# Optimization experiments

Hardware: AMD Instinct MI355X
Metric: run time of the kernel (lower is better)

The kernel has to match this reference:

```python
import jax, jax.numpy as jnp
import numpy as np


def setup_inputs() -> dict:
    key = jax.random.key(0)
    kq, kk, kv = jax.random.split(key, 3)
    B, S, D = 4, 4096, 128
    return {
        "q_proj": jax.random.normal(kq, (B, S, D), dtype=jnp.float32),
        "k_proj": jax.random.normal(kk, (B, S, D), dtype=jnp.float32),
        "v_proj": jax.random.normal(kv, (B, S, D), dtype=jnp.float32),
    }


def reference(q_proj, k_proj, v_proj):
    # Block-wise online softmax in the original is mathematically exact
    # full (non-causal) scaled dot-product attention.
    d = q_proj.shape[-1]
    scale = 1.0 / jnp.sqrt(jnp.asarray(d, dtype=q_proj.dtype))
    logits = jnp.einsum('bqd,bkd->bqk', q_proj, k_proj) * scale  # [B,S,S]
    attn = jax.nn.softmax(logits, axis=-1)
    return jnp.einsum('bqk,bkd->bqd', attn, v_proj)
```

## Files before the change

### kernel.cpp

```cpp
#include <hip/hip_runtime.h>
#include <hip/hip_bf16.h>
#include <stdint.h>

#define Bn 4
#define Sn 4096
#define Dn 128
#define SCALE ((float)(0.08838834764831843 * 1.4426950408889634))

typedef __attribute__((ext_vector_type(8)))  short short8;
typedef __attribute__((ext_vector_type(4)))  short short4v;
typedef __attribute__((ext_vector_type(4)))  float f32x4;
typedef __attribute__((ext_vector_type(16))) float f32x16;
typedef __attribute__((ext_vector_type(2)))  uint32_t uint2v;

__device__ __forceinline__ uint32_t bfround(float f){
  union { float f; uint32_t u; } a; a.f = f;
  return a.u + 0x7FFFu + ((a.u >> 16) & 1u);
}
__device__ __forceinline__ uint32_t f2bf2(float lo, float hi){
  return (bfround(hi) & 0xFFFF0000u) | (bfround(lo) >> 16);
}
__device__ __forceinline__ uint32_t f2bf2_fast(float lo, float hi){
  const uint32_t a = __float_as_uint(lo) + 0x8000u;
  const uint32_t b = __float_as_uint(hi) + 0x8000u;
  return __builtin_amdgcn_perm(b, a, 0x07060302u);
}
__device__ __forceinline__ float bf2f(short s){
  union { uint32_t u; float f; } a; a.u = ((uint32_t)(unsigned short)s) << 16; return a.f;
}
__device__ __forceinline__ float fexp2(float x){
#if __has_builtin(__builtin_amdgcn_exp2f)
  return __builtin_amdgcn_exp2f(x);
#else
  return exp2f(x);
#endif
}

__device__ __forceinline__ void gload16(const void* g, void* l){
  __builtin_amdgcn_global_load_lds(
      (const __attribute__((address_space(1))) unsigned int*)g,
      (__attribute__((address_space(3))) unsigned int*)l, 16, 0, 0);
}

__global__ void prep_kernel(const float* __restrict__ k, const float* __restrict__ v,
                            short* __restrict__ kb, short* __restrict__ vt){
  const int bid = blockIdx.x;
  const int t   = threadIdx.x;
  if (bid < 2048){
    const int i = bid*256 + t;
    const f32x4 val = ((const f32x4*)k)[i];
    uint2v o;
    o[0] = f2bf2(val[0], val[1]);
    o[1] = f2bf2(val[2], val[3]);
    *(uint2v*)(kb + 4*(size_t)i) = o;
  } else {
    __shared__ float tile[64][65];
    const int vb = bid - 2048;
    const int s0 = (vb & 63) * 64;
    const int d0 = ((vb >> 6) & 1) * 64;
    const int b  = vb >> 7;
#pragma unroll
    for (int i=0;i<16;++i){
      int lin = i*256 + t;
      int r = lin >> 6, c = lin & 63;
      tile[r][c] = v[((size_t)(b*Sn + s0 + r))*Dn + d0 + c];
    }
    __syncthreads();
#pragma unroll
    for (int i=0;i<2;++i){
      int lin = i*256 + t;
      int r = lin >> 3;
      int u = lin & 7;
      union { uint32_t w[4]; short8 s; } pk;
#pragma unroll
      for (int p=0;p<4;++p){
        int x0 = u*8 + 2*p, x1 = x0 + 1;
        int k0 = (x0 & ~15) | ((x0 & 3) | (((x0>>2)&1)<<3) | (((x0>>3)&1)<<2));
        int k1 = (x1 & ~15) | ((x1 & 3) | (((x1>>2)&1)<<3) | (((x1>>3)&1)<<2));
        pk.w[p] = f2bf2(tile[k0][r], tile[k1][r]);
      }
      *(short8*)(vt + ((size_t)(b*Dn + d0 + r))*Sn + s0 + u*8) = pk.s;
    }
  }
}

__global__ __launch_bounds__(256, 3) void fa_kernel(
    const float* __restrict__ Qg, const short* __restrict__ Kb,
    const short* __restrict__ VTb, short* __restrict__ parts,
    float* __restrict__ lparts){
  __shared__ __align__(16) char lds[32768];
  const int tid = threadIdx.x;
  const int w = tid >> 6, lane = tid & 63;
  const int ln = lane & 31, h5 = lane >> 5;
  const int idx = blockIdx.x;
  const int b   = idx & 3;
  const int u2  = idx >> 2;
  const int qt  = u2 & 31;
  const int ks  = u2 >> 5;
  const int q0  = qt * 128;
  const int start_it = ks*21 + (ks < 2 ? ks : 2);
  const int n_it     = 21 + (ks < 2 ? 1 : 0);

  short8 Qf[8];
  {
    const float* qp = Qg + ((size_t)(b*Sn + q0 + w*32 + ln))*Dn;
#pragma unroll
    for (int t=0;t<8;++t){
      const int d0 = t*16 + h5*8;
      const f32x4 a = *(const f32x4*)(qp + d0);
      const f32x4 c = *(const f32x4*)(qp + d0 + 4);
      union { uint32_t u[4]; short8 s; } pk;
      pk.u[0] = f2bf2(a[0]*SCALE, a[1]*SCALE);
      pk.u[1] = f2bf2(a[2]*SCALE, a[3]*SCALE);
      pk.u[2] = f2bf2(c[0]*SCALE, c[1]*SCALE);
      pk.u[3] = f2bf2(c[2]*SCALE, c[3]*SCALE);
      Qf[t] = pk.s;
    }
  }

  f32x16 Ot[4];
#pragma unroll
  for (int m=0;m<4;++m)
#pragma unroll
    for (int r=0;r<16;++r) Ot[m][r] = 0.0f;
  float ls0=0.f, ls1=0.f, ls2=0.f, ls3=0.f;

  int goff[4], loff[4];
  const char* gbase;
  if (w < 2){
#pragma unroll
    for (int i=0;i<4;++i){
      const int ch = i*128 + w*64 + lane;
      const int r  = ch >> 4;
      const int gc = (ch & 15) ^ (r & 7);
      goff[i] = r*256 + gc*16;
      loff[i] = ch*16;
    }
    gbase = (const char*)Kb + ((size_t)(b*Sn + start_it*32))*256;
  } else {
#pragma unroll
    for (int i=0;i<4;++i){
      const int ch = i*128 + (w-2)*64 + lane;
      const int r  = ch >> 2;
      const int gc = (ch & 3) ^ ((r >> 1) & 3);
      goff[i] = r*8192 + gc*16;
      loff[i] = 8192 + ch*16;
    }
    gbase = (const char*)VTb + (size_t)b*Dn*Sn*2 + (size_t)start_it*64;
  }

  auto stage = [&](int i, int ph){
    char* ldsb = lds + ph*16384;
    const char* gb = gbase + (w < 2 ? (size_t)i*8192 : (size_t)i*64);
#pragma unroll
    for (int u=0;u<4;++u) gload16(gb + goff[u], ldsb + loff[u]);
  };

  stage(0, 0);

  for (int i=0; i<n_it; ++i){
    const int ph = i & 1;
    __syncthreads();
    if (i+1 < n_it) stage(i+1, ph^1);

    const char* bK = lds + ph*16384;
    const char* bV = bK + 8192;

    f32x16 St;
#pragma unroll
    for (int r=0;r<16;++r) St[r] = 0.0f;
#pragma unroll
    for (int t=0;t<8;++t){
      const int pos = ((2*t + h5) ^ (ln & 7)) * 16;
      const short8 kf = *(const short8*)(bK + (size_t)ln*256 + pos);
      St = __builtin_amdgcn_mfma_f32_32x32x16_bf16(kf, Qf[t], St, 0, 0, 0);
    }

#pragma unroll
    for (int r=0;r<16;++r) St[r] = fexp2(St[r]);
#pragma unroll
    for (int r=0;r<16;r+=4){
      ls0 += St[r]; ls1 += St[r+1]; ls2 += St[r+2]; ls3 += St[r+3];
    }

#pragma unroll
    for (int t=0;t<2;++t){
      union { uint32_t u[4]; short8 s; } pf;
      pf.u[0] = f2bf2_fast(St[8*t+0], St[8*t+1]);
      pf.u[1] = f2bf2_fast(St[8*t+2], St[8*t+3]);
      pf.u[2] = f2bf2_fast(St[8*t+4], St[8*t+5]);
      pf.u[3] = f2bf2_fast(St[8*t+6], St[8*t+7]);
      const int phys = ((2*t + h5) ^ ((ln >> 1) & 3)) * 16;
#pragma unroll
      for (int mt=0;mt<4;++mt){
        const short8 vf = *(const short8*)(bV + (size_t)(mt*32+ln)*64 + phys);
        Ot[mt] = __builtin_amdgcn_mfma_f32_32x32x16_bf16(vf, pf.s, Ot[mt], 0, 0, 0);
      }
    }
  }

  float lsum = (ls0 + ls1) + (ls2 + ls3);
  lsum += __shfl_xor(lsum, 32, 64);

  const int pslot = (b*32 + qt)*6 + ks;
  short* pbase = parts + (size_t)pslot*16384 + (size_t)(w*32 + ln)*128;
#pragma unroll
  for (int mt=0;mt<4;++mt){
#pragma unroll
    for (int g=0;g<4;++g){
      union { uint32_t u[2]; short4v s; } o;
      o.u[0] = f2bf2(Ot[mt][4*g],   Ot[mt][4*g+1]);
      o.u[1] = f2bf2(Ot[mt][4*g+2], Ot[mt][4*g+3]);
      *(short4v*)(pbase + mt*32 + 8*g + 4*h5) = o.s;
    }
  }
  if (h5 == 0) lparts[(size_t)pslot*128 + w*32 + ln] = lsum;
}

__global__ void reduce_kernel(const short* __restrict__ parts,
                              const float* __restrict__ lparts,
                              float* __restrict__ out){
  const int t  = threadIdx.x;
  const int s  = blockIdx.x >> 3;
  const int qg = (blockIdx.x & 7)*16 + (t >> 4);
  const int d0 = (t & 15) * 8;
  float acc[8];
#pragma unroll
  for (int j=0;j<8;++j) acc[j] = 0.0f;
  float lsum = 0.0f;
#pragma unroll
  for (int ks=0;ks<6;++ks){
    const short8 p = *(const short8*)(parts + ((size_t)(s*6+ks))*16384 + (size_t)qg*128 + d0);
#pragma unroll
    for (int j=0;j<8;++j) acc[j] += bf2f(p[j]);
    lsum += lparts[(size_t)(s*6+ks)*128 + qg];
  }
  const float linv = 1.0f / lsum;
  f32x4 o0, o1;
#pragma unroll
  for (int j=0;j<4;++j){ o0[j] = acc[j]*linv; o1[j] = acc[4+j]*linv; }
  float* op = out + ((size_t)(s*128 + qg))*128 + d0;
  *(f32x4*)op = o0;
  *(f32x4*)(op + 4) = o1;
}

extern "C" void kernel_launch(void* const* d_in, const int* in_sizes, int n_in,
                              void* d_out, int out_size, void* d_ws, size_t ws_size,
                              hipStream_t stream){
  const float* q = (const float*)d_in[0];
  const float* k = (const float*)d_in[1];
  const float* v = (const float*)d_in[2];
  float* out = (float*)d_out;
  char* ws = (char*)d_ws;
  short* kb     = (short*)ws;
  short* vt     = kb + (size_t)Bn*Sn*Dn;
  short* parts  = (short*)(ws + 8388608);
  float* lparts = (float*)(ws + 8388608 + 25165824);

  prep_kernel<<<2560, 256, 0, stream>>>(k, v, kb, vt);
  fa_kernel<<<768, 256, 0, stream>>>(q, kb, vt, parts, lparts);
  reduce_kernel<<<1024, 256, 0, stream>>>(parts, lparts, out);
}
```

Baseline: 121.8 us.

## Pre-swizzle K/V into MFMA fragment layout and load directly to registers

The prep kernel now writes K and V in the exact per-lane MFMA fragment order, so the attention kernel reads fragments straight from global memory into registers. This drops the LDS double-buffering, the global_load_lds staging and the per-iteration __syncthreads. The key-split assignment across blocks is also reordered. The cost is that each of the four waves loads the full K/V tile independently, relying on L2/L1 instead of shared LDS, and the exposed load latency is no longer hidden by an async prefetch stage.

```diff
diff --git a/kernel.cpp b/kernel.cpp
--- a/kernel.cpp
+++ b/kernel.cpp
@@ -11,7 +11,6 @@
 typedef __attribute__((ext_vector_type(4)))  short short4v;
 typedef __attribute__((ext_vector_type(4)))  float f32x4;
 typedef __attribute__((ext_vector_type(16))) float f32x16;
-typedef __attribute__((ext_vector_type(2)))  uint32_t uint2v;
 
 __device__ __forceinline__ uint32_t bfround(float f){
   union { float f; uint32_t u; } a; a.f = f;
@@ -35,71 +34,90 @@
   return exp2f(x);
 #endif
 }
-
-__device__ __forceinline__ void gload16(const void* g, void* l){
-  __builtin_amdgcn_global_load_lds(
-      (const __attribute__((address_space(1))) unsigned int*)g,
-      (__attribute__((address_space(3))) unsigned int*)l, 16, 0, 0);
+__device__ __forceinline__ int bitswap23(int x){
+  return (x & ~15) | ((x & 3) | (((x>>2)&1)<<3) | (((x>>3)&1)<<2));
 }
 
 __global__ void prep_kernel(const float* __restrict__ k, const float* __restrict__ v,
-                            short* __restrict__ kb, short* __restrict__ vt){
+                            short* __restrict__ kf, short* __restrict__ vf){
   const int bid = blockIdx.x;
-  const int t   = threadIdx.x;
-  if (bid < 2048){
-    const int i = bid*256 + t;
-    const f32x4 val = ((const f32x4*)k)[i];
-    uint2v o;
-    o[0] = f2bf2(val[0], val[1]);
-    o[1] = f2bf2(val[2], val[3]);
-    *(uint2v*)(kb + 4*(size_t)i) = o;
+  const int tid = threadIdx.x;
+  if (bid < 512){
+    const int b  = bid >> 7, kt = bid & 127;
+#pragma unroll
+    for (int i=0;i<2;++i){
+      const int idx = i*256 + tid;
+      const int t = idx >> 6, lane = idx & 63;
+      const int ln = lane & 31, h5 = lane >> 5;
+      const float* src = k + ((size_t)(b*Sn + kt*32 + ln))*Dn + t*16 + h5*8;
+      const f32x4 a = *(const f32x4*)src;
+      const f32x4 c = *(const f32x4*)(src + 4);
+      union { uint32_t u[4]; short8 s; } pk;
+      pk.u[0] = f2bf2(a[0], a[1]);
+      pk.u[1] = f2bf2(a[2], a[3]);
+      pk.u[2] = f2bf2(c[0], c[1]);
+      pk.u[3] = f2bf2(c[2], c[3]);
+      *(short8*)(kf + ((((size_t)(b*128 + kt))*8 + t)*64 + lane)*8) = pk.s;
+    }
   } else {
     __shared__ float tile[64][65];
-    const int vb = bid - 2048;
-    const int s0 = (vb & 63) * 64;
-    const int d0 = ((vb >> 6) & 1) * 64;
-    const int b  = vb >> 7;
+    const int vb  = bid - 512;
+    const int b   = vb >> 7;
+    const int rem = vb & 127;
+    const int s0t = rem & 63;
+    const int d0t = rem >> 6;
+    const int s0 = s0t*64, d0 = d0t*64;
 #pragma unroll
     for (int i=0;i<16;++i){
-      int lin = i*256 + t;
+      int lin = i*256 + tid;
       int r = lin >> 6, c = lin & 63;
       tile[r][c] = v[((size_t)(b*Sn + s0 + r))*Dn + d0 + c];
     }
     __syncthreads();
 #pragma unroll
     for (int i=0;i<2;++i){
-      int lin = i*256 + t;
-      int r = lin >> 3;
-      int u = lin & 7;
-      union { uint32_t w[4]; short8 s; } pk;
+      const int idx = i*256 + tid;
+      const int g = idx >> 6, lane = idx & 63;
+      const int ln = lane & 31, h5 = lane >> 5;
+      const int kt_l = g >> 2, t = (g >> 1) & 1, mt_l = g & 1;
+      const int kt = s0t*2 + kt_l;
+      const int mt = d0t*2 + mt_l;
+      const int c  = 2*t + h5;
+      const int dl = mt_l*32 + ln;
+      union { uint32_t u[4]; short8 s; } pk;
+#pragma unroll
+      for (int p=0;p<2;++p){
+        const int x0 = c*8 + 2*p*2;
+      }
 #pragma unroll
       for (int p=0;p<4;++p){
-        int x0 = u*8 + 2*p, x1 = x0 + 1;
-        int k0 = (x0 & ~15) | ((x0 & 3) | (((x0>>2)&1)<<3) | (((x0>>3)&1)<<2));
-        int k1 = (x1 & ~15) | ((x1 & 3) | (((x1>>2)&1)<<3) | (((x1>>3)&1)<<2));
-        pk.w[p] = f2bf2(tile[k0][r], tile[k1][r]);
+        const int x0 = c*8 + 2*p, x1 = x0 + 1;
+        const int k0 = kt_l*32 + bitswap23(x0);
+        const int k1 = kt_l*32 + bitswap23(x1);
+        pk.u[p] = f2bf2(tile[k0][dl], tile[k1][dl]);
       }
-      *(short8*)(vt + ((size_t)(b*Dn + d0 + r))*Sn + s0 + u*8) = pk.s;
+      *(short8*)(vf + ((((size_t)(b*128 + kt))*8 + t*4 + mt)*64 + lane)*8) = pk.s;
     }
   }
 }
 
 __global__ __launch_bounds__(256, 3) void fa_kernel(
-    const float* __restrict__ Qg, const short* __restrict__ Kb,
-    const short* __restrict__ VTb, short* __restrict__ parts,
+    const float* __restrict__ Qg, const short* __restrict__ KF,
+    const short* __restrict__ VF, short* __restrict__ parts,
     float* __restrict__ lparts){
-  __shared__ __align__(16) char lds[32768];
   const int tid = threadIdx.x;
   const int w = tid >> 6, lane = tid & 63;
   const int ln = lane & 31, h5 = lane >> 5;
   const int idx = blockIdx.x;
-  const int b   = idx & 3;
-  const int u2  = idx >> 2;
-  const int qt  = u2 & 31;
-  const int ks  = u2 >> 5;
-  const int q0  = qt * 128;
-  const int start_it = ks*21 + (ks < 2 ? ks : 2);
-  const int n_it     = 21 + (ks < 2 ? 1 : 0);
+  const int b     = idx & 3;
+  const int khalf = (idx >> 2) & 1;
+  const int r     = idx >> 3;
+  const int qt    = r & 31;
+  const int kk    = r >> 5;
+  const int ksIdx = khalf*3 + kk;
+  const int q0    = qt * 128;
+  const int start_kt = khalf*64 + (kk == 0 ? 0 : 22 + 21*(kk-1));
+  const int n_it     = (kk == 0 ? 22 : 21);
 
   short8 Qf[8];
   {
@@ -122,65 +140,32 @@
 #pragma unroll
   for (int m=0;m<4;++m)
 #pragma unroll
-    for (int r=0;r<16;++r) Ot[m][r] = 0.0f;
+    for (int rr=0;rr<16;++rr) Ot[m][rr] = 0.0f;
   float ls0=0.f, ls1=0.f, ls2=0.f, ls3=0.f;
 
-  int goff[4], loff[4];
-  const char* gbase;
-  if (w < 2){
-#pragma unroll
-    for (int i=0;i<4;++i){
-      const int ch = i*128 + w*64 + lane;
-      const int r  = ch >> 4;
-      const int gc = (ch & 15) ^ (r & 7);
-      goff[i] = r*256 + gc*16;
-      loff[i] = ch*16;
-    }
-    gbase = (const char*)Kb + ((size_t)(b*Sn + start_it*32))*256;
-  } else {
-#pragma unroll
-    for (int i=0;i<4;++i){
-      const int ch = i*128 + (w-2)*64 + lane;
-      const int r  = ch >> 2;
-      const int gc = (ch & 3) ^ ((r >> 1) & 3);
-      goff[i] = r*8192 + gc*16;
-      loff[i] = 8192 + ch*16;
-    }
-    gbase = (const char*)VTb + (size_t)b*Dn*Sn*2 + (size_t)start_it*64;
-  }
-
-  auto stage = [&](int i, int ph){
-    char* ldsb = lds + ph*16384;
-    const char* gb = gbase + (w < 2 ? (size_t)i*8192 : (size_t)i*64);
-#pragma unroll
-    for (int u=0;u<4;++u) gload16(gb + goff[u], ldsb + loff[u]);
-  };
-
-  stage(0, 0);
+  const short* kfp = KF + (((size_t)(b*128 + start_kt))*8)*512 + (size_t)lane*8;
+  const short* vfp = VF + (((size_t)(b*128 + start_kt))*8)*512 + (size_t)lane*8;
 
   for (int i=0; i<n_it; ++i){
-    const int ph = i & 1;
-    __syncthreads();
-    if (i+1 < n_it) stage(i+1, ph^1);
-
-    const char* bK = lds + ph*16384;
-    const char* bV = bK + 8192;
-
+    short8 kf[8];
+#pragma unroll
+    for (int t=0;t<8;++t) kf[t] = *(const short8*)(kfp + (size_t)t*512);
     f32x16 St;
 #pragma unroll
-    for (int r=0;r<16;++r) St[r] = 0.0f;
-#pragma unroll
-    for (int t=0;t<8;++t){
-      const int pos = ((2*t + h5) ^ (ln & 7)) * 16;
-      const short8 kf = *(const short8*)(bK + (size_t)ln*256 + pos);
-      St = __builtin_amdgcn_mfma_f32_32x32x16_bf16(kf, Qf[t], St, 0, 0, 0);
-    }
-
-#pragma unroll
-    for (int r=0;r<16;++r) St[r] = fexp2(St[r]);
-#pragma unroll
-    for (int r=0;r<16;r+=4){
-      ls0 += St[r]; ls1 += St[r+1]; ls2 += St[r+2]; ls3 += St[r+3];
+    for (int rr=0;rr<16;++rr) St[rr] = 0.0f;
+#pragma unroll
+    for (int t=0;t<8;++t)
+      St = __builtin_amdgcn_mfma_f32_32x32x16_bf16(kf[t], Qf[t], St, 0, 0, 0);
+
+    short8 vfr[8];
+#pragma unroll
+    for (int u=0;u<8;++u) vfr[u] = *(const short8*)(vfp + (size_t)u*512);
+
+#pragma unroll
+    for (int rr=0;rr<16;++rr) St[rr] = fexp2(St[rr]);
+#pragma unroll
+    for (int rr=0;rr<16;rr+=4){
+      ls0 += St[rr]; ls1 += St[rr+1]; ls2 += St[rr+2]; ls3 += St[rr+3];
     }
 
 #pragma unroll
@@ -190,19 +175,19 @@
       pf.u[1] = f2bf2_fast(St[8*t+2], St[8*t+3]);
       pf.u[2] = f2bf2_fast(St[8*t+4], St[8*t+5]);
       pf.u[3] = f2bf2_fast(St[8*t+6], St[8*t+7]);
-      const int phys = ((2*t + h5) ^ ((ln >> 1) & 3)) * 16;
-#pragma unroll
-      for (int mt=0;mt<4;++mt){
-        const short8 vf = *(const short8*)(bV + (size_t)(mt*32+ln)*64 + phys);
-        Ot[mt] = __builtin_amdgcn_mfma_f32_32x32x16_bf16(vf, pf.s, Ot[mt], 0, 0, 0);
-      }
-    }
+#pragma unroll
+      for (int mt=0;mt<4;++mt)
+        Ot[mt] = __builtin_amdgcn_mfma_f32_32x32x16_bf16(vfr[t*4+mt], pf.s, Ot[mt], 0, 0, 0);
+    }
+
+    kfp += 8*512;
+    vfp += 8*512;
   }
 
   float lsum = (ls0 + ls1) + (ls2 + ls3);
   lsum += __shfl_xor(lsum, 32, 64);
 
-  const int pslot = (b*32 + qt)*6 + ks;
+  const int pslot = (b*32 + qt)*6 + ksIdx;
   short* pbase = parts + (size_t)pslot*16384 + (size_t)(w*32 + ln)*128;
 #pragma unroll
   for (int mt=0;mt<4;++mt){
@@ -252,12 +237,12 @@
   const float* v = (const float*)d_in[2];
   float* out = (float*)d_out;
   char* ws = (char*)d_ws;
-  short* kb     = (short*)ws;
-  short* vt     = kb + (size_t)Bn*Sn*Dn;
+  short* kfb    = (short*)ws;
+  short* vfb    = kfb + (size_t)Bn*Sn*Dn;
   short* parts  = (short*)(ws + 8388608);
   float* lparts = (float*)(ws + 8388608 + 25165824);
 
-  prep_kernel<<<2560, 256, 0, stream>>>(k, v, kb, vt);
-  fa_kernel<<<768, 256, 0, stream>>>(q, kb, vt, parts, lparts);
+  prep_kernel<<<1024, 256, 0, stream>>>(k, v, kfb, vfb);
+  fa_kernel<<<768, 256, 0, stream>>>(q, kfb, vfb, parts, lparts);
   reduce_kernel<<<1024, 256, 0, stream>>>(parts, lparts, out);
 }
```

Result: slower. 128.4 us (+5.4%).
